# Optimization experiments

Hardware: AMD Instinct MI355X
Metric: run time of the kernel (lower is better)

Reference implementation:

```python
import jax, jax.numpy as jnp
import numpy as np

N_NODES = 50000
N_EDGES = 800000
D = 128

def setup_inputs() -> dict:
    key = jax.random.key(0)
    k1, k2, k3, k4 = jax.random.split(key, 4)
    x = jax.random.normal(k1, (N_NODES, D), dtype=jnp.float32)
    edge_index = jax.random.randint(k2, (2, N_EDGES), 0, N_NODES, dtype=jnp.int64)
    # nn.Linear params: W is (out_dim, in_dim), b is (out_dim,)
    W = jax.random.normal(k3, (D, D), dtype=jnp.float32) * (1.0 / np.sqrt(D))
    b = jax.random.normal(k4, (D,), dtype=jnp.float32) * 0.01
    return {"x": x, "edge_index": edge_index, "W": W, "b": b}

def reference(x, edge_index, W, b):
    row, col = edge_index[0], edge_index[1]
    h = x @ W.T + b                      # (N, D) linear projection
    msgs = h[col]                        # gather by source col, (E, D)
    agg = jax.ops.segment_sum(msgs, row, num_segments=N_NODES)  # scatter-add by row
    return agg + h                       # residual
```

## Files before the change

### kernel.cpp

```cpp
#include <hip/hip_runtime.h>

#define NN 50000
#define NE 800000
#define DD 128
#define TILE_M 64
#define CAP 64

#define NBG ((NN + TILE_M - 1) / TILE_M)
#define ECHUNK 2048
#define NCH ((NE + ECHUNK - 1) / ECHUNK)
#define NBS (NCH * 8)

typedef __attribute__((ext_vector_type(8))) short short8;
typedef __attribute__((ext_vector_type(4))) float f32x4;

__device__ __forceinline__ unsigned short f2bf(float f) {
    unsigned int u = __float_as_uint(f);
    u += 0x7fffu + ((u >> 16) & 1u);
    return (unsigned short)(u >> 16);
}

__global__ __launch_bounds__(256) void prologue(
    const float* __restrict__ W, unsigned short* __restrict__ Wbf,
    int* __restrict__ deg)
{
    const int t = blockIdx.x * 256 + threadIdx.x;
    for (int i = t; i < NN; i += 64 * 256) deg[i] = 0;
    if (blockIdx.x == 0) {
        for (int i = threadIdx.x; i < 128 * 32; i += 256) {
            const float4 w4 = ((const float4*)W)[i];
            ushort4 s4;
            s4.x = f2bf(w4.x); s4.y = f2bf(w4.y);
            s4.z = f2bf(w4.z); s4.w = f2bf(w4.w);
            *(ushort4*)(Wbf + i * 4) = s4;
        }
    }
}

__global__ __launch_bounds__(256, 6) void fused_gemm_scatter(
    const float* __restrict__ x, const unsigned short* __restrict__ Wbf,
    const float* __restrict__ b, const int* __restrict__ ei,
    float* __restrict__ out, unsigned short* __restrict__ hbf,
    int* __restrict__ deg, int* __restrict__ slots)
{
    if (blockIdx.x >= NBG) {
        const int part  = blockIdx.x & 7;
        const int chunk = (blockIdx.x - NBG) >> 3;
        const int base  = chunk * ECHUNK;
#pragma unroll
        for (int i = 0; i < 8; ++i) {
            const int e = base + i * 256 + threadIdx.x;
            if (e < NE) {
                const int r = ei[e];
                if (((r >> 4) & 7) == part) {
                    const int c = ei[NE + e];
                    const int p = atomicAdd(&deg[r], 1);
                    if (p < CAP) slots[r * CAP + p] = c;
                }
            }
        }
        return;
    }

    const int t    = threadIdx.x;
    const int lane = t & 63;
    const int wave = t >> 6;
    const int m16  = lane & 15;
    const int quad = lane >> 4;

    const int row0 = blockIdx.x * TILE_M;
    int gr = row0 + wave * 16 + m16;
    if (gr > NN - 1) gr = NN - 1;

    short8 afrag[4];
#pragma unroll
    for (int kc = 0; kc < 4; ++kc) {
        const float4 a0 = *(const float4*)(x + (size_t)gr * 128 + kc * 32 + quad * 8);
        const float4 a1 = *(const float4*)(x + (size_t)gr * 128 + kc * 32 + quad * 8 + 4);
        short8 af;
        af[0] = (short)f2bf(a0.x); af[1] = (short)f2bf(a0.y);
        af[2] = (short)f2bf(a0.z); af[3] = (short)f2bf(a0.w);
        af[4] = (short)f2bf(a1.x); af[5] = (short)f2bf(a1.y);
        af[6] = (short)f2bf(a1.z); af[7] = (short)f2bf(a1.w);
        afrag[kc] = af;
    }

    f32x4 acc[8];
#pragma unroll
    for (int nt = 0; nt < 8; ++nt) acc[nt] = (f32x4){0.f, 0.f, 0.f, 0.f};

#pragma unroll
    for (int kc = 0; kc < 4; ++kc) {
#pragma unroll
        for (int nt = 0; nt < 8; ++nt) {
            const short8 bfrag =
                *(const short8*)(Wbf + (nt * 16 + m16) * 128 + kc * 32 + quad * 8);
            acc[nt] = __builtin_amdgcn_mfma_f32_16x16x32_bf16(
                afrag[kc], bfrag, acc[nt], 0, 0, 0);
        }
    }

    const int rbase = row0 + wave * 16 + quad * 4;
#pragma unroll
    for (int nt = 0; nt < 8; ++nt) {
        const float bias = b[nt * 16 + m16];
#pragma unroll
        for (int r = 0; r < 4; ++r) {
            const int grow = rbase + r;
            if (grow < NN) {
                const float v = acc[nt][r] + bias;
                out[(size_t)grow * 128 + nt * 16 + m16] = v;
                hbf[(size_t)grow * 128 + nt * 16 + m16] = f2bf(v);
            }
        }
    }
}

__global__ __launch_bounds__(256) void agg_kernel(
    const int* __restrict__ deg, const int* __restrict__ slots,
    const unsigned short* __restrict__ hbf, float* __restrict__ out)
{
    const int n = (blockIdx.x * 256 + threadIdx.x) >> 6;
    if (n >= NN) return;
    const int lane = threadIdx.x & 63;
    const int g = lane >> 4;
    const int s = lane & 15;

    const int dn_raw = deg[n];
    const int idx    = slots[n * CAP + lane];
    float4 r0, r1;
    if (g == 0) {
        r0 = *(const float4*)(out + (size_t)n * 128 + s * 8);
        r1 = *(const float4*)(out + (size_t)n * 128 + s * 8 + 4);
    }
    const int dn = min(dn_raw, CAP);

    float acc[8];
#pragma unroll
    for (int i = 0; i < 8; ++i) acc[i] = 0.f;

    for (int k = 0; k < dn; k += 16) {
        uint4 p[4];
#pragma unroll
        for (int bb = 0; bb < 4; ++bb) {
            const int e = k + bb * 4 + g;
            const int c = __shfl(idx, e, 64);
            p[bb] = (uint4){0u, 0u, 0u, 0u};
            if (e < dn)
                p[bb] = *(const uint4*)(hbf + (size_t)c * 128 + s * 8);
        }
#pragma unroll
        for (int bb = 0; bb < 4; ++bb) {
            acc[0] += __uint_as_float(p[bb].x << 16);
            acc[1] += __uint_as_float(p[bb].x & 0xffff0000u);
            acc[2] += __uint_as_float(p[bb].y << 16);
            acc[3] += __uint_as_float(p[bb].y & 0xffff0000u);
            acc[4] += __uint_as_float(p[bb].z << 16);
            acc[5] += __uint_as_float(p[bb].z & 0xffff0000u);
            acc[6] += __uint_as_float(p[bb].w << 16);
            acc[7] += __uint_as_float(p[bb].w & 0xffff0000u);
        }
    }

#pragma unroll
    for (int i = 0; i < 8; ++i) acc[i] += __shfl_xor(acc[i], 16, 64);
#pragma unroll
    for (int i = 0; i < 8; ++i) acc[i] += __shfl_xor(acc[i], 32, 64);

    if (g == 0) {
        r0.x += acc[0]; r0.y += acc[1]; r0.z += acc[2]; r0.w += acc[3];
        r1.x += acc[4]; r1.y += acc[5]; r1.z += acc[6]; r1.w += acc[7];
        *(float4*)(out + (size_t)n * 128 + s * 8)     = r0;
        *(float4*)(out + (size_t)n * 128 + s * 8 + 4) = r1;
    }
}

extern "C" void kernel_launch(void* const* d_in, const int* in_sizes, int n_in,
                              void* d_out, int out_size, void* d_ws, size_t ws_size,
                              hipStream_t stream)
{
    const float* x  = (const float*)d_in[0];
    const int*   ei = (const int*)d_in[1];
    const float* W  = (const float*)d_in[2];
    const float* b  = (const float*)d_in[3];
    float* out = (float*)d_out;

    unsigned short* hbf   = (unsigned short*)d_ws;
    int*            slots = (int*)(hbf + (size_t)NN * DD);
    int*            deg   = slots + (size_t)NN * CAP;
    unsigned short* Wbf   = (unsigned short*)(deg + NN);

    prologue<<<64, 256, 0, stream>>>(W, Wbf, deg);

    fused_gemm_scatter<<<NBG + NBS, 256, 0, stream>>>(x, Wbf, b, ei, out, hbf, deg, slots);

    agg_kernel<<<(NN * 64 + 255) / 256, 256, 0, stream>>>(deg, slots, hbf, out);
}
```

Measured before the change: 163.6 us.

## Split fused GEMM/scatter into separate kernels and mask slot loads by degree

Replaces the single launch, which ran GEMM tiles and edge-scatter blocks side by side, with two launches: a simple one-edge-per-thread scatter kernel and a standalone GEMM kernel. The scatter no longer splits edges into 8 row partitions, so each edge index is read once instead of by 8 blocks, but atomics to the same row are no longer grouped. The aggregation kernel now skips loading slot entries past the node's degree, which avoids reading uninitialized slots. The split gives up the overlap between GEMM and scatter and adds a launch.

```diff
diff --git a/kernel.cpp b/kernel.cpp
--- a/kernel.cpp
+++ b/kernel.cpp
@@ -7,9 +7,7 @@
 #define CAP 64
 
 #define NBG ((NN + TILE_M - 1) / TILE_M)
-#define ECHUNK 2048
-#define NCH ((NE + ECHUNK - 1) / ECHUNK)
-#define NBS (NCH * 8)
+#define NBS ((NE + 255) / 256)
 
 typedef __attribute__((ext_vector_type(8))) short short8;
 typedef __attribute__((ext_vector_type(4))) float f32x4;
@@ -37,31 +35,23 @@
     }
 }
 
-__global__ __launch_bounds__(256, 6) void fused_gemm_scatter(
+__global__ __launch_bounds__(256) void scatter_kernel(
+    const int* __restrict__ ei, int* __restrict__ deg, int* __restrict__ slots)
+{
+    const int e = blockIdx.x * 256 + threadIdx.x;
+    if (e < NE) {
+        const int r = ei[e];
+        const int c = ei[NE + e];
+        const int p = atomicAdd(&deg[r], 1);
+        if (p < CAP) slots[r * CAP + p] = c;
+    }
+}
+
+__global__ __launch_bounds__(256, 6) void gemm_kernel(
     const float* __restrict__ x, const unsigned short* __restrict__ Wbf,
-    const float* __restrict__ b, const int* __restrict__ ei,
-    float* __restrict__ out, unsigned short* __restrict__ hbf,
-    int* __restrict__ deg, int* __restrict__ slots)
+    const float* __restrict__ b, float* __restrict__ out,
+    unsigned short* __restrict__ hbf)
 {
-    if (blockIdx.x >= NBG) {
-        const int part  = blockIdx.x & 7;
-        const int chunk = (blockIdx.x - NBG) >> 3;
-        const int base  = chunk * ECHUNK;
-#pragma unroll
-        for (int i = 0; i < 8; ++i) {
-            const int e = base + i * 256 + threadIdx.x;
-            if (e < NE) {
-                const int r = ei[e];
-                if (((r >> 4) & 7) == part) {
-                    const int c = ei[NE + e];
-                    const int p = atomicAdd(&deg[r], 1);
-                    if (p < CAP) slots[r * CAP + p] = c;
-                }
-            }
-        }
-        return;
-    }
-
     const int t    = threadIdx.x;
     const int lane = t & 63;
     const int wave = t >> 6;
@@ -127,13 +117,13 @@
     const int s = lane & 15;
 
     const int dn_raw = deg[n];
-    const int idx    = slots[n * CAP + lane];
+    const int dn = min(dn_raw, CAP);
+    const int idx = (lane < dn) ? slots[n * CAP + lane] : 0;
     float4 r0, r1;
     if (g == 0) {
         r0 = *(const float4*)(out + (size_t)n * 128 + s * 8);
         r1 = *(const float4*)(out + (size_t)n * 128 + s * 8 + 4);
     }
-    const int dn = min(dn_raw, CAP);
 
     float acc[8];
 #pragma unroll
@@ -192,7 +182,9 @@
 
     prologue<<<64, 256, 0, stream>>>(W, Wbf, deg);
 
-    fused_gemm_scatter<<<NBG + NBS, 256, 0, stream>>>(x, Wbf, b, ei, out, hbf, deg, slots);
+    scatter_kernel<<<NBS, 256, 0, stream>>>(ei, deg, slots);
+
+    gemm_kernel<<<NBG, 256, 0, stream>>>(x, Wbf, b, out, hbf);
 
     agg_kernel<<<(NN * 64 + 255) / 256, 256, 0, stream>>>(deg, slots, hbf, out);
 }
```

Result: slower. 181.7 us (+11.0%).
